# Optimization experiments

Hardware: AMD Instinct MI355X
Metric: run time of the kernel (lower is better)

## Reference

```python
import jax, jax.numpy as jnp
import numpy as np

MARGIN = 2.0


def setup_inputs() -> dict:
    key = jax.random.key(0)
    k1, k2 = jax.random.split(key)
    B, D, NUM_CLASSES = 8192, 128, 100
    features = jax.random.normal(k1, (B, D), dtype=jnp.float32)
    labels = jax.random.randint(k2, (B,), 0, NUM_CLASSES, dtype=jnp.int64)
    return {"features": features, "labels": labels}


def reference(features, labels):
    # Vectorized form of the O(B^2) nested-loop contrastive loss.
    B = features.shape[0]
    sq = jnp.sum(features * features, axis=-1)                      # [B]
    # squared pairwise L2 distances via the gram matrix
    d2 = sq[:, None] + sq[None, :] - 2.0 * (features @ features.T)  # [B, B]
    d2 = jnp.maximum(d2, 0.0)

    off_diag = ~jnp.eye(B, dtype=bool)
    same = labels[:, None] == labels[None, :]
    pos_mask = same & off_diag
    neg_mask = (~same) & off_diag

    # positive pairs contribute squared distance
    pos_loss = jnp.sum(jnp.where(pos_mask, d2, 0.0))

    # negative pairs contribute clamp(margin - dist, 0)^2; guard sqrt(0) grads
    d = jnp.sqrt(jnp.where(neg_mask, d2, 1.0))
    hinge = jnp.maximum(MARGIN - d, 0.0)
    neg_loss = jnp.sum(jnp.where(neg_mask, hinge * hinge, 0.0))

    pos_count = jnp.sum(pos_mask)
    total_pairs = jnp.asarray(B * (B - 1), dtype=d2.dtype)
    loss = pos_loss + neg_loss
    # original divides only when positive_pairs > 0
    return jnp.where(pos_count > 0, loss / total_pairs, loss)
```

## Files before the change

### kernel.cpp

```cpp
#include <hip/hip_runtime.h>
#include <hip/hip_bf16.h>


#define BN 8192
#define DD 128
#define NTILES 64
#define NBLOCKS (NTILES * (NTILES + 1) / 2)
#define LS 136

typedef __attribute__((ext_vector_type(8))) short bf16x8;
typedef __attribute__((ext_vector_type(4))) float f32x4;

__global__ __launch_bounds__(256) void prep_kernel(const float* __restrict__ f,
        const int* __restrict__ labels, short* __restrict__ fbp,
        float2* __restrict__ meta) {
    const int tid = threadIdx.x;
    const int p = blockIdx.x;
    __shared__ unsigned short ls[16][LS];

    const int r = tid >> 4;
    const int c = (tid & 15) * 8;
    const float* src = f + ((size_t)p * 16 + r) * DD + c;
    float4 a = *(const float4*)src;
    float4 b = *(const float4*)(src + 4);
    float rv[8] = {a.x, a.y, a.z, a.w, b.x, b.y, b.z, b.w};
    float s = 0.f;
#pragma unroll
    for (int j = 0; j < 8; j++) {
        __hip_bfloat16 h = __float2bfloat16(rv[j]);
        ls[r][c + j] = *(unsigned short*)&h;
        float rr = __bfloat162float(h);
        s = fmaf(rr, rr, s);
    }
#pragma unroll
    for (int off = 8; off > 0; off >>= 1) s += __shfl_down(s, off, 16);
    if ((tid & 15) == 0) meta[p * 16 + r] = make_float2(s, (float)labels[p * 16 + r]);
    __syncthreads();

    const int w = tid >> 6, lane = tid & 63;
    const int l15 = lane & 15, quad = lane >> 4;
    bf16x8 pack = *(const bf16x8*)&ls[l15][w * 32 + quad * 8];
    *(bf16x8*)(fbp + ((size_t)(p * 4 + w) * 64 + lane) * 8) = pack;
}

__global__ __launch_bounds__(256, 4) void pair_kernel(
        const short* __restrict__ fbp, const float2* __restrict__ meta,
        float2* __restrict__ partial) {
    const int t = blockIdx.x;
    int by = (int)((sqrtf(8.f * (float)t + 1.f) - 1.f) * 0.5f);
    while ((by + 1) * (by + 2) / 2 <= t) by++;
    while (by * (by + 1) / 2 > t) by--;
    const int bx = t - by * (by + 1) / 2;
    const bool diag = (bx == by);

    const int tid = threadIdx.x;
    const int wave = tid >> 6, lane = tid & 63;
    const int wx = wave & 1, wy = wave >> 1;
    const int i0 = bx * 128 + wy * 64;
    const int j0 = by * 128 + wx * 64;
    const int ip = i0 >> 4, jp = j0 >> 4;
    const int l15 = lane & 15, quad = lane >> 4;

    float pos = 0.f, neg = 0.f;

    if (!(diag && wx < wy)) {
        f32x4 acc4[4][4];
#pragma unroll
        for (int a = 0; a < 4; a++)
#pragma unroll
            for (int b = 0; b < 4; b++) acc4[a][b] = (f32x4){0.f, 0.f, 0.f, 0.f};

#pragma unroll
        for (int ks = 0; ks < 4; ks++) {
            bf16x8 af[4], bg[4];
#pragma unroll
            for (int tt = 0; tt < 4; tt++)
                af[tt] = *(const bf16x8*)(fbp +
                    ((size_t)((ip + tt) * 4 + ks) * 64 + lane) * 8);
#pragma unroll
            for (int tt = 0; tt < 4; tt++)
                bg[tt] = *(const bf16x8*)(fbp +
                    ((size_t)((jp + tt) * 4 + ks) * 64 + lane) * 8);
#pragma unroll
            for (int m = 0; m < 4; m++)
#pragma unroll
                for (int n = 0; n < 4; n++)
                    acc4[m][n] = __builtin_amdgcn_mfma_f32_16x16x32_bf16(
                        af[m], bg[n], acc4[m][n], 0, 0, 0);
        }

        float2 mj[4];
#pragma unroll
        for (int ni = 0; ni < 4; ni++) mj[ni] = meta[j0 + ni * 16 + l15];
        float2 mi[4][4];
#pragma unroll
        for (int m = 0; m < 4; m++)
#pragma unroll
            for (int r = 0; r < 4; r++) mi[m][r] = meta[i0 + m * 16 + quad * 4 + r];

        const bool strict = diag && (wx == wy);
#pragma unroll
        for (int m = 0; m < 4; m++)
#pragma unroll
            for (int n = 0; n < 4; n++)
#pragma unroll
                for (int r = 0; r < 4; r++) {
                    int il = m * 16 + quad * 4 + r;
                    int jl = n * 16 + l15;
                    bool valid = !strict || (il < jl);
                    float d2 = fmaxf(mi[m][r].x + mj[n].x - 2.f * acc4[m][n][r], 0.f);
                    if (valid) {
                        if (mi[m][r].y == mj[n].y) pos += d2;
                        else if (d2 < 4.0f) {
                            float h = 2.0f - sqrtf(d2);
                            neg += h * h;
                        }
                    }
                }
    }

#pragma unroll
    for (int off = 32; off > 0; off >>= 1) {
        pos += __shfl_down(pos, off, 64);
        neg += __shfl_down(neg, off, 64);
    }
    __shared__ float red[2][4];
    if (lane == 0) { red[0][wave] = pos; red[1][wave] = neg; }
    __syncthreads();
    if (tid == 0)
        partial[t] = make_float2(red[0][0] + red[0][1] + red[0][2] + red[0][3],
                                 red[1][0] + red[1][1] + red[1][2] + red[1][3]);
}

__global__ __launch_bounds__(256) void reduce_kernel(
        const float2* __restrict__ partial, float* __restrict__ out) {
    const int tid = threadIdx.x;
    float p = 0.f, n = 0.f;
    for (int i = tid; i < NBLOCKS; i += 256) {
        float2 v = partial[i];
        p += v.x; n += v.y;
    }
#pragma unroll
    for (int off = 32; off > 0; off >>= 1) {
        p += __shfl_down(p, off, 64);
        n += __shfl_down(n, off, 64);
    }
    __shared__ float red[2][4];
    int lane = tid & 63, w = tid >> 6;
    if (lane == 0) { red[0][w] = p; red[1][w] = n; }
    __syncthreads();
    if (tid == 0) {
        float total = 2.0f * (red[0][0] + red[0][1] + red[0][2] + red[0][3] +
                              red[1][0] + red[1][1] + red[1][2] + red[1][3]);
        out[0] = total / 67100672.0f;
    }
}

extern "C" void kernel_launch(void* const* d_in, const int* in_sizes, int n_in,
                              void* d_out, int out_size, void* d_ws, size_t ws_size,
                              hipStream_t stream) {
    const float* f = (const float*)d_in[0];
    const int* labels = (const int*)d_in[1];
    float* out = (float*)d_out;

    short* fbp = (short*)d_ws;
    float2* meta = (float2*)((char*)d_ws + (size_t)BN * DD * sizeof(short));
    float2* partial = meta + BN;

    prep_kernel<<<BN / 16, 256, 0, stream>>>(f, labels, fbp, meta);
    pair_kernel<<<NBLOCKS, 256, 0, stream>>>(fbp, meta, partial);
    reduce_kernel<<<1, 256, 0, stream>>>(partial, out);
}
```

Baseline: 87.63 us.

## Stage row tile in LDS and sweep four column tiles per block with prefetch

Each block now keeps its 128-row A tile resident in shared memory and walks up to four consecutive column tiles, prefetching the next B fragments into registers while the current tile's epilogue runs. The triangular tile index decode is replaced by a 2D grid of row tile by chunk, where out-of-range chunks write zero partials. The aim is to cut repeated global loads of A and hide B load latency. In exchange, occupancy drops to 2 blocks per CU, registers rise from the double-buffered B fragments, and many blocks in the grid exit immediately.

```diff
diff --git a/kernel.cpp b/kernel.cpp
--- a/kernel.cpp
+++ b/kernel.cpp
@@ -5,7 +5,8 @@
 #define BN 8192
 #define DD 128
 #define NTILES 64
-#define NBLOCKS (NTILES * (NTILES + 1) / 2)
+#define NCHUNK 16
+#define NBLK (NTILES * NCHUNK)
 #define LS 136
 
 typedef __attribute__((ext_vector_type(8))) short bf16x8;
@@ -43,80 +44,118 @@
     *(bf16x8*)(fbp + ((size_t)(p * 4 + w) * 64 + lane) * 8) = pack;
 }
 
-__global__ __launch_bounds__(256, 4) void pair_kernel(
+__global__ __launch_bounds__(256, 2) void pair_kernel(
         const short* __restrict__ fbp, const float2* __restrict__ meta,
         float2* __restrict__ partial) {
-    const int t = blockIdx.x;
-    int by = (int)((sqrtf(8.f * (float)t + 1.f) - 1.f) * 0.5f);
-    while ((by + 1) * (by + 2) / 2 <= t) by++;
-    while (by * (by + 1) / 2 > t) by--;
-    const int bx = t - by * (by + 1) / 2;
-    const bool diag = (bx == by);
-
+    const int ti = blockIdx.x;
+    const int ch = blockIdx.y;
+    const int slot = ti * NCHUNK + ch;
+    const int j0 = ti + ch * 4;
     const int tid = threadIdx.x;
+
+    if (j0 >= NTILES) {
+        if (tid == 0) partial[slot] = make_float2(0.f, 0.f);
+        return;
+    }
+    const int jend = min(j0 + 3, NTILES - 1);
+
     const int wave = tid >> 6, lane = tid & 63;
     const int wx = wave & 1, wy = wave >> 1;
-    const int i0 = bx * 128 + wy * 64;
-    const int j0 = by * 128 + wx * 64;
-    const int ip = i0 >> 4, jp = j0 >> 4;
     const int l15 = lane & 15, quad = lane >> 4;
+    const int i0 = ti * 128 + wy * 64;
+
+    __shared__ char atile[32768];
+    {
+        const char* srcA = (const char*)fbp + (size_t)ti * 32768;
+#pragma unroll
+        for (int q = 0; q < 8; q++)
+            *(float4*)(atile + q * 4096 + tid * 16) =
+                *(const float4*)(srcA + q * 4096 + tid * 16);
+    }
+    float2 mi[4][4];
+#pragma unroll
+    for (int m = 0; m < 4; m++)
+#pragma unroll
+        for (int r = 0; r < 4; r++) mi[m][r] = meta[i0 + m * 16 + quad * 4 + r];
+    __syncthreads();
 
     float pos = 0.f, neg = 0.f;
 
-    if (!(diag && wx < wy)) {
+    auto loadB = [&](int tj, bf16x8* bg, float2* mj) {
+        const int pb = tj * 8 + wx * 4;
+#pragma unroll
+        for (int tt = 0; tt < 4; tt++)
+#pragma unroll
+            for (int ks = 0; ks < 4; ks++)
+                bg[tt * 4 + ks] = *(const bf16x8*)(fbp +
+                    ((size_t)((pb + tt) * 4 + ks) * 64 + lane) * 8);
+        const int jb = tj * 128 + wx * 64;
+#pragma unroll
+        for (int n = 0; n < 4; n++) mj[n] = meta[jb + n * 16 + l15];
+    };
+
+    bf16x8 bg[16]; float2 mj[4];
+    loadB(j0, bg, mj);
+
+#pragma unroll
+    for (int s = 0; s < 4; s++) {
+        const int jt = j0 + s;
+        if (jt > jend) break;
+        const bool diagstep = (jt == ti);
+        const bool active = !(diagstep && wx < wy);
+        const bool strict = diagstep && (wx == wy);
+
         f32x4 acc4[4][4];
 #pragma unroll
         for (int a = 0; a < 4; a++)
 #pragma unroll
             for (int b = 0; b < 4; b++) acc4[a][b] = (f32x4){0.f, 0.f, 0.f, 0.f};
 
-#pragma unroll
-        for (int ks = 0; ks < 4; ks++) {
-            bf16x8 af[4], bg[4];
-#pragma unroll
-            for (int tt = 0; tt < 4; tt++)
-                af[tt] = *(const bf16x8*)(fbp +
-                    ((size_t)((ip + tt) * 4 + ks) * 64 + lane) * 8);
-#pragma unroll
-            for (int tt = 0; tt < 4; tt++)
-                bg[tt] = *(const bf16x8*)(fbp +
-                    ((size_t)((jp + tt) * 4 + ks) * 64 + lane) * 8);
+        if (active) {
+#pragma unroll
+            for (int ks = 0; ks < 4; ks++) {
+                bf16x8 af[4];
+#pragma unroll
+                for (int tt = 0; tt < 4; tt++)
+                    af[tt] = *(const bf16x8*)(atile +
+                        (((wy * 4 + tt) * 4 + ks) << 10) + lane * 16);
+#pragma unroll
+                for (int m = 0; m < 4; m++)
+#pragma unroll
+                    for (int n = 0; n < 4; n++)
+                        acc4[m][n] = __builtin_amdgcn_mfma_f32_16x16x32_bf16(
+                            af[m], bg[n * 4 + ks], acc4[m][n], 0, 0, 0);
+            }
+        }
+
+        bf16x8 bn[16]; float2 mjn[4];
+        if (jt + 1 <= jend) loadB(jt + 1, bn, mjn);
+
+        if (active) {
 #pragma unroll
             for (int m = 0; m < 4; m++)
 #pragma unroll
                 for (int n = 0; n < 4; n++)
-                    acc4[m][n] = __builtin_amdgcn_mfma_f32_16x16x32_bf16(
-                        af[m], bg[n], acc4[m][n], 0, 0, 0);
-        }
-
-        float2 mj[4];
-#pragma unroll
-        for (int ni = 0; ni < 4; ni++) mj[ni] = meta[j0 + ni * 16 + l15];
-        float2 mi[4][4];
-#pragma unroll
-        for (int m = 0; m < 4; m++)
-#pragma unroll
-            for (int r = 0; r < 4; r++) mi[m][r] = meta[i0 + m * 16 + quad * 4 + r];
-
-        const bool strict = diag && (wx == wy);
-#pragma unroll
-        for (int m = 0; m < 4; m++)
-#pragma unroll
-            for (int n = 0; n < 4; n++)
-#pragma unroll
-                for (int r = 0; r < 4; r++) {
-                    int il = m * 16 + quad * 4 + r;
-                    int jl = n * 16 + l15;
-                    bool valid = !strict || (il < jl);
-                    float d2 = fmaxf(mi[m][r].x + mj[n].x - 2.f * acc4[m][n][r], 0.f);
-                    if (valid) {
-                        if (mi[m][r].y == mj[n].y) pos += d2;
-                        else if (d2 < 4.0f) {
-                            float h = 2.0f - sqrtf(d2);
-                            neg += h * h;
+#pragma unroll
+                    for (int r = 0; r < 4; r++) {
+                        int il = m * 16 + quad * 4 + r;
+                        int jl = n * 16 + l15;
+                        bool valid = !strict || (il < jl);
+                        float d2 = fmaxf(mi[m][r].x + mj[n].x - 2.f * acc4[m][n][r], 0.f);
+                        if (valid) {
+                            if (mi[m][r].y == mj[n].y) pos += d2;
+                            else if (d2 < 4.0f) {
+                                float h = 2.0f - sqrtf(d2);
+                                neg += h * h;
+                            }
                         }
                     }
-                }
+        }
+
+#pragma unroll
+        for (int q = 0; q < 16; q++) bg[q] = bn[q];
+#pragma unroll
+        for (int n = 0; n < 4; n++) mj[n] = mjn[n];
     }
 
 #pragma unroll
@@ -128,15 +167,15 @@
     if (lane == 0) { red[0][wave] = pos; red[1][wave] = neg; }
     __syncthreads();
     if (tid == 0)
-        partial[t] = make_float2(red[0][0] + red[0][1] + red[0][2] + red[0][3],
-                                 red[1][0] + red[1][1] + red[1][2] + red[1][3]);
+        partial[slot] = make_float2(red[0][0] + red[0][1] + red[0][2] + red[0][3],
+                                    red[1][0] + red[1][1] + red[1][2] + red[1][3]);
 }
 
 __global__ __launch_bounds__(256) void reduce_kernel(
         const float2* __restrict__ partial, float* __restrict__ out) {
     const int tid = threadIdx.x;
     float p = 0.f, n = 0.f;
-    for (int i = tid; i < NBLOCKS; i += 256) {
+    for (int i = tid; i < NBLK; i += 256) {
         float2 v = partial[i];
         p += v.x; n += v.y;
     }
@@ -168,6 +207,7 @@
     float2* partial = meta + BN;
 
     prep_kernel<<<BN / 16, 256, 0, stream>>>(f, labels, fbp, meta);
-    pair_kernel<<<NBLOCKS, 256, 0, stream>>>(fbp, meta, partial);
+    dim3 grid(NTILES, NCHUNK);
+    pair_kernel<<<grid, 256, 0, stream>>>(fbp, meta, partial);
     reduce_kernel<<<1, 256, 0, stream>>>(partial, out);
 }
```

After: 105.6 us. 1.21x slower.
